# Optimization experiments

Hardware: AMD Instinct MI355X
Metric: run time of the kernel (lower is better)

Reference implementation:

```python
import jax, jax.numpy as jnp
import numpy as np

N = 200_000   # nodes
E = 6_400_000 # edges (avg degree 32)
G = 1024      # graphs in the batch
H = 8         # hidden dim


def setup_inputs() -> dict:
    key = jax.random.key(0)
    ks = jax.random.split(key, 13)
    x = jax.random.normal(ks[0], (N, 1), dtype=jnp.float32)
    edge_index = jax.random.randint(ks[1], (2, E), 0, N, dtype=jnp.int32)
    batch = jnp.sort(jax.random.randint(ks[2], (N,), 0, G, dtype=jnp.int32))
    s = 0.3
    params = dict(
        W1a=s * jax.random.normal(ks[3], (1, H), jnp.float32),
        b1a=jnp.zeros((H,), jnp.float32),
        W1b=s * jax.random.normal(ks[4], (H, H), jnp.float32),
        b1b=jnp.zeros((H,), jnp.float32),
        W2a=s * jax.random.normal(ks[5], (H, H), jnp.float32),
        b2a=jnp.zeros((H,), jnp.float32),
        W2b=s * jax.random.normal(ks[6], (H, H), jnp.float32),
        b2b=jnp.zeros((H,), jnp.float32),
        Wfc=s * jax.random.normal(ks[7], (H, 1), jnp.float32),
        bfc=jnp.zeros((1,), jnp.float32),
    )
    return dict(x=x, edge_index=edge_index, batch=batch, **params)


def _gin_layer(h, src, dst, Wa, ba, Wb, bb):
    # GINConv with eps=0: mlp(x_i + sum_{j->i} x_j); messages aggregated at dst=edge_index[1]
    agg = jax.ops.segment_sum(h[src], dst, num_segments=N)  # [N, d]
    z = h + agg
    z = jax.nn.relu(z @ Wa + ba)
    return z @ Wb + bb


def reference(x, edge_index, batch, W1a, b1a, W1b, b1b, W2a, b2a, W2b, b2b, Wfc, bfc):
    src, dst = edge_index[0], edge_index[1]
    h = _gin_layer(x, src, dst, W1a, b1a, W1b, b1b)   # [N, 8]
    h = jax.nn.elu(h)
    h = _gin_layer(h, src, dst, W2a, b2a, W2b, b2b)   # [N, 8]
    # global mean pool over graphs
    sums = jax.ops.segment_sum(h, batch, num_segments=G)                  # [G, 8]
    counts = jax.ops.segment_sum(jnp.ones((N,), h.dtype), batch, num_segments=G)
    pooled = sums / jnp.maximum(counts, 1.0)[:, None]
    out = jax.nn.sigmoid(pooled @ Wfc + bfc)          # [G, 1]
    return out.reshape(-1)
```

## Files before the change

### kernel.cpp

```cpp
#include <hip/hip_runtime.h>
#include <hip/hip_fp8.h>
#include <math.h>

#define H 8
#define NBLKA 256
#define BTH 1024
#define BSH 8
#define BCAP 9216
#define TS 1024
#define CAP 14336
#define SCAP 25600
#define POOLG 128

__device__ __forceinline__ unsigned f2fp8(float f) {
    __hip_fp8_e4m3 q(f);
    return (unsigned)q.__x;
}
__device__ __forceinline__ float fp8f(unsigned v) {
    __hip_fp8_e4m3 q;
    q.__x = (__hip_fp8_storage_t)v;
    return (float)q;
}
__device__ __forceinline__ void acc8(float* a, uint2 v) {
    a[0] += fp8f(v.x & 255u);         a[1] += fp8f((v.x >> 8) & 255u);
    a[2] += fp8f((v.x >> 16) & 255u); a[3] += fp8f(v.x >> 24);
    a[4] += fp8f(v.y & 255u);         a[5] += fp8f((v.y >> 8) & 255u);
    a[6] += fp8f((v.y >> 16) & 255u); a[7] += fp8f(v.y >> 24);
}

__global__ __launch_bounds__(BTH) void scatterK(const int* __restrict__ ei, int E, int NB,
                                                int chunk, int* __restrict__ cursor,
                                                unsigned* __restrict__ packed) {
    __shared__ unsigned ss[SCAP];
    __shared__ int cnt[1024], sc[1024], base[1024], cur[1024];
    int t = threadIdx.x, blk = blockIdx.x;
    cnt[t] = 0;
    __syncthreads();
    int s = blk * chunk, e = min(E, s + chunk);
    for (int i = s + t; i < e; i += BTH)
        atomicAdd(&cnt[__builtin_nontemporal_load(ei + E + i) >> BSH], 1);
    __syncthreads();
    int c = cnt[t];
    sc[t] = c;
    __syncthreads();
    for (int off = 1; off < 1024; off <<= 1) {
        int v = (t >= off) ? sc[t - off] : 0;
        __syncthreads();
        sc[t] += v;
        __syncthreads();
    }
    cur[t] = sc[t] - c;
    base[t] = (t < NB && c > 0) ? atomicAdd(&cursor[t], c) : 0;
    __syncthreads();
    for (int i = s + t; i < e; i += BTH) {
        int src = __builtin_nontemporal_load(ei + i);
        int dst = __builtin_nontemporal_load(ei + E + i);
        int pos = atomicAdd(&cur[dst >> BSH], 1);
        ss[pos] = ((unsigned)src << 8) | (unsigned)(dst & 255);
    }
    __syncthreads();
    int wave = t >> 6, lane = t & 63;
    for (int j = wave; j < NB; j += (BTH >> 6)) {
        int n = cnt[j];
        int ls = sc[j] - n;
        int bs = base[j];
        int m = min(n, BCAP - bs);
        int gs = j * BCAP + bs;
        for (int k = lane; k < m; k += 64)
            packed[gs + k] = ss[ls + k];
    }
}

__global__ void sortL1K(unsigned* __restrict__ packed, const int* __restrict__ bucketCnt,
                        const float* __restrict__ x, int N,
                        const float* __restrict__ W1a, const float* __restrict__ b1a,
                        const float* __restrict__ W1b, const float* __restrict__ b1b,
                        int* __restrict__ nodeStart, uint2* __restrict__ h1) {
    __shared__ unsigned ss[CAP];
    __shared__ int cnt[256], sb[256], cur[256];
    __shared__ float sW1a[H], sb1a[H], sW1b[H * H], sb1b[H];
    int t = threadIdx.x, b = blockIdx.x;
    if (t < 256) cnt[t] = 0;
    else if (t < 256 + H) { int j = t - 256; sW1a[j] = W1a[j]; sb1a[j] = b1a[j]; sb1b[j] = b1b[j]; }
    else if (t < 256 + H + H * H) { int j = t - 256 - H; sW1b[j] = W1b[j]; }
    __syncthreads();
    int s = b * BCAP;
    int n_e = min(bucketCnt[b], BCAP);
    for (int i = t; i < n_e; i += TS)
        atomicAdd(&cnt[__builtin_nontemporal_load(packed + s + i) & 255u], 1);
    __syncthreads();
    if (t < 256) sb[t] = cnt[t];
    __syncthreads();
    for (int off = 1; off < 256; off <<= 1) {
        int add = (t < 256 && t >= off) ? sb[t - off] : 0;
        __syncthreads();
        if (t < 256) sb[t] += add;
        __syncthreads();
    }
    if (t < 256) {
        int excl = sb[t] - cnt[t];
        cur[t] = excl;
        nodeStart[(b << BSH) + t] = s + excl;
    }
    __syncthreads();
    for (int i = t; i < n_e; i += TS) {
        unsigned p = __builtin_nontemporal_load(packed + s + i);
        int pos = atomicAdd(&cur[p & 255u], 1);
        ss[pos] = p >> 8;
    }
    __syncthreads();
    for (int i = t; i < n_e; i += TS) packed[s + i] = ss[i];
    int node = t >> 2, q4 = t & 3;
    int gn = (b << BSH) + node;
    int lo = sb[node] - cnt[node], hi = sb[node];
    float sum = 0.f;
    for (int k = lo + q4; k < hi; k += 16) {
        int k1 = k + 4, k2 = k + 8, k3 = k + 12;
        unsigned i0 = ss[k];
        unsigned i1 = ss[min(k1, hi - 1)];
        unsigned i2 = ss[min(k2, hi - 1)];
        unsigned i3 = ss[min(k3, hi - 1)];
        float x0 = x[i0], x1 = x[i1], x2 = x[i2], x3 = x[i3];
        sum += x0;
        if (k1 < hi) sum += x1;
        if (k2 < hi) sum += x2;
        if (k3 < hi) sum += x3;
    }
    sum += __shfl_xor(sum, 1, 64);
    sum += __shfl_xor(sum, 2, 64);
    if (q4 == 0 && gn < N) {
        float z = x[gn] + sum;
        float tv[H];
#pragma unroll
        for (int k = 0; k < H; k++) tv[k] = fmaxf(fmaf(z, sW1a[k], sb1a[k]), 0.f);
        float hv[H];
#pragma unroll
        for (int j = 0; j < H; j++) {
            float a = sb1b[j];
#pragma unroll
            for (int k = 0; k < H; k++) a += tv[k] * sW1b[k * H + j];
            hv[j] = a > 0.f ? a : (expf(a) - 1.f);
        }
        uint2 o;
        o.x = f2fp8(hv[0]) | (f2fp8(hv[1]) << 8) | (f2fp8(hv[2]) << 16) | (f2fp8(hv[3]) << 24);
        o.y = f2fp8(hv[4]) | (f2fp8(hv[5]) << 8) | (f2fp8(hv[6]) << 16) | (f2fp8(hv[7]) << 24);
        h1[gn] = o;
    }
}

__global__ __launch_bounds__(1024) void layer2K(
        const unsigned* __restrict__ packed, const int* __restrict__ nodeStart,
        const int* __restrict__ bucketCnt, const uint2* __restrict__ h1, int N,
        const float* __restrict__ W2a, const float* __restrict__ b2a,
        const float* __restrict__ W2b, const float* __restrict__ b2b,
        const int* __restrict__ batch, float* __restrict__ sumsCnt) {
    __shared__ unsigned ss[BCAP];
    __shared__ int sNS[257];
    __shared__ float pool[POOLG * 9];
    __shared__ float sW2a[H * H], sb2a[H], sW2b[H * H], sb2b[H];
    int t = threadIdx.x, b = blockIdx.x;
    int s = b * BCAP;
    int n_e = min(bucketCnt[b], BCAP);
    for (int i = t; i < n_e; i += 1024)
        ss[i] = __builtin_nontemporal_load(packed + s + i);
    if (t < 256) sNS[t] = nodeStart[(b << BSH) + t] - s;
    if (t == 256) sNS[256] = 0;
    if (t < H) { sb2a[t] = b2a[t]; sb2b[t] = b2b[t]; }
    else if (t >= 64 && t < 64 + H * H) sW2a[t - 64] = W2a[t - 64];
    else if (t >= 192 && t < 192 + H * H) sW2b[t - 192] = W2b[t - 192];
    __syncthreads();
    if (t == 0) sNS[256] = n_e;
    __syncthreads();
    int node = t >> 2, q4 = t & 3;
    int gn = (b << BSH) + node;
    int lo = sNS[node], hi = sNS[node + 1];
    float a[H] = {0.f, 0.f, 0.f, 0.f, 0.f, 0.f, 0.f, 0.f};
    for (int k = lo + q4; k < hi; k += 16) {
        int k1 = k + 4, k2 = k + 8, k3 = k + 12;
        unsigned i0 = ss[k];
        unsigned i1 = ss[min(k1, hi - 1)];
        unsigned i2 = ss[min(k2, hi - 1)];
        unsigned i3 = ss[min(k3, hi - 1)];
        uint2 v0 = h1[i0];
        uint2 v1 = h1[i1];
        uint2 v2 = h1[i2];
        uint2 v3 = h1[i3];
        acc8(a, v0);
        if (k1 < hi) acc8(a, v1);
        if (k2 < hi) acc8(a, v2);
        if (k3 < hi) acc8(a, v3);
    }
#pragma unroll
    for (int j = 0; j < H; j++) {
        a[j] += __shfl_xor(a[j], 1, 64);
        a[j] += __shfl_xor(a[j], 2, 64);
    }
    bool valid = (q4 == 0) && (gn < N);
    float h2[H];
    int g = 0;
    if (valid) {
        uint2 v = h1[gn];
        float z[H] = {fp8f(v.x & 255u) + a[0],         fp8f((v.x >> 8) & 255u) + a[1],
                      fp8f((v.x >> 16) & 255u) + a[2], fp8f(v.x >> 24) + a[3],
                      fp8f(v.y & 255u) + a[4],         fp8f((v.y >> 8) & 255u) + a[5],
                      fp8f((v.y >> 16) & 255u) + a[6], fp8f(v.y >> 24) + a[7]};
        float tv[H];
#pragma unroll
        for (int k = 0; k < H; k++) {
            float acc = sb2a[k];
#pragma unroll
            for (int j = 0; j < H; j++) acc += z[j] * sW2a[j * H + k];
            tv[k] = fmaxf(acc, 0.f);
        }
#pragma unroll
        for (int j = 0; j < H; j++) {
            float acc = sb2b[j];
#pragma unroll
            for (int k = 0; k < H; k++) acc += tv[k] * sW2b[k * H + j];
            h2[j] = acc;
        }
        g = batch[gn];
    }
    int gfirst = batch[min(b << BSH, N - 1)];
    int glast  = batch[min((b << BSH) + 255, N - 1)];
    int span = glast - gfirst + 1;
    if (span <= POOLG) {
        int span9 = span * 9;
        for (int j = t; j < span9; j += 1024) pool[j] = 0.f;
        __syncthreads();
        if (valid) {
            float* p = &pool[(g - gfirst) * 9];
#pragma unroll
            for (int j = 0; j < H; j++) atomicAdd(p + j, h2[j]);
            atomicAdd(p + 8, 1.f);
        }
        __syncthreads();
        for (int j = t; j < span9; j += 1024)
            atomicAdd(&sumsCnt[(size_t)gfirst * 9 + j], pool[j]);
    } else if (valid) {
        float* p = &sumsCnt[(size_t)g * 9];
#pragma unroll
        for (int j = 0; j < H; j++) atomicAdd(p + j, h2[j]);
        atomicAdd(p + 8, 1.f);
    }
}

__global__ void finalK(const float* __restrict__ sumsCnt, const float* __restrict__ Wfc,
                       const float* __restrict__ bfc, float* __restrict__ out, int G) {
    int g = blockIdx.x * blockDim.x + threadIdx.x;
    if (g >= G) return;
    const float* s = &sumsCnt[(size_t)g * 9];
    float c = fmaxf(s[8], 1.f);
    float dot = 0.f;
#pragma unroll
    for (int j = 0; j < H; j++) dot += s[j] * Wfc[j];
    float a = dot / c + bfc[0];
    out[g] = 1.f / (1.f + expf(-a));
}

__global__ void edge_agg1(const int* __restrict__ ei, const float* __restrict__ x,
                          float* __restrict__ agg1, int E) {
    int e = blockIdx.x * blockDim.x + threadIdx.x;
    if (e >= E) return;
    atomicAdd(&agg1[ei[E + e]], x[ei[e]]);
}
__global__ void node1F(const float* __restrict__ x, const float* __restrict__ agg1,
                       const float* __restrict__ W1a, const float* __restrict__ b1a,
                       const float* __restrict__ W1b, const float* __restrict__ b1b,
                       float* __restrict__ h1, int N) {
    int n = blockIdx.x * blockDim.x + threadIdx.x;
    if (n >= N) return;
    float z = x[n] + agg1[n];
    float tv[H];
#pragma unroll
    for (int k = 0; k < H; k++) tv[k] = fmaxf(z * W1a[k] + b1a[k], 0.f);
#pragma unroll
    for (int j = 0; j < H; j++) {
        float acc = b1b[j];
#pragma unroll
        for (int k = 0; k < H; k++) acc += tv[k] * W1b[k * H + j];
        h1[(size_t)n * H + j] = acc > 0.f ? acc : (expf(acc) - 1.f);
    }
}
__global__ void edge_agg2(const int* __restrict__ ei, const float* __restrict__ h1,
                          float* __restrict__ agg2, int E) {
    long long i = (long long)blockIdx.x * blockDim.x + threadIdx.x;
    if (i >= (long long)E * H) return;
    int e = (int)(i >> 3), k = (int)(i & 7);
    atomicAdd(&agg2[(size_t)ei[E + e] * H + k], h1[(size_t)ei[e] * H + k]);
}
__global__ void node2F(const float* __restrict__ h1, const float* __restrict__ agg2,
                       const float* __restrict__ W2a, const float* __restrict__ b2a,
                       const float* __restrict__ W2b, const float* __restrict__ b2b,
                       const int* __restrict__ batch,
                       float* __restrict__ sums, float* __restrict__ counts, int N) {
    int n = blockIdx.x * blockDim.x + threadIdx.x;
    if (n >= N) return;
    float z[H], tv[H];
#pragma unroll
    for (int j = 0; j < H; j++) z[j] = h1[(size_t)n * H + j] + agg2[(size_t)n * H + j];
#pragma unroll
    for (int k = 0; k < H; k++) {
        float a = b2a[k];
#pragma unroll
        for (int j = 0; j < H; j++) a += z[j] * W2a[j * H + k];
        tv[k] = fmaxf(a, 0.f);
    }
    int g = batch[n];
#pragma unroll
    for (int j = 0; j < H; j++) {
        float a = b2b[j];
#pragma unroll
        for (int k = 0; k < H; k++) a += tv[k] * W2b[k * H + j];
        atomicAdd(&sums[(size_t)g * H + j], a);
    }
    atomicAdd(&counts[g], 1.f);
}
__global__ void finalF(const float* __restrict__ sums, const float* __restrict__ counts,
                       const float* __restrict__ Wfc, const float* __restrict__ bfc,
                       float* __restrict__ out, int G) {
    int g = blockIdx.x * blockDim.x + threadIdx.x;
    if (g >= G) return;
    float c = fmaxf(counts[g], 1.f);
    float acc = bfc[0];
#pragma unroll
    for (int j = 0; j < H; j++) acc += (sums[(size_t)g * H + j] / c) * Wfc[j];
    out[g] = 1.f / (1.f + expf(-acc));
}

extern "C" void kernel_launch(void* const* d_in, const int* in_sizes, int n_in,
                              void* d_out, int out_size, void* d_ws, size_t ws_size,
                              hipStream_t stream) {
    const float* x    = (const float*)d_in[0];
    const int*   ei   = (const int*)d_in[1];
    const int*   batch= (const int*)d_in[2];
    const float* W1a  = (const float*)d_in[3];
    const float* b1a  = (const float*)d_in[4];
    const float* W1b  = (const float*)d_in[5];
    const float* b1b  = (const float*)d_in[6];
    const float* W2a  = (const float*)d_in[7];
    const float* b2a  = (const float*)d_in[8];
    const float* W2b  = (const float*)d_in[9];
    const float* b2b  = (const float*)d_in[10];
    const float* Wfc  = (const float*)d_in[11];
    const float* bfc  = (const float*)d_in[12];

    const int N = in_sizes[0];
    const int E = in_sizes[1] / 2;
    const int G = out_size;
    const int NB = (N + 255) >> BSH;
    const int chunk = (E + NBLKA - 1) / NBLKA;
    const int B = 256;

    auto rnd4 = [](size_t v) { return (v + 3) & ~(size_t)3; };
    size_t o_cur  = 0;
    size_t o_sc   = 1024;
    size_t zelems = o_sc + (size_t)9 * G;
    size_t o_ns   = rnd4(zelems);
    size_t o_h1   = rnd4(o_ns + ((size_t)NB << BSH) + 1);
    size_t o_pk   = rnd4(o_h1 + ((size_t)NB << BSH) * 2);
    size_t total  = o_pk + (size_t)NB * BCAP;

    bool srcFits = (N <= (1 << 18));
    bool chunkFits = (chunk <= SCAP);
    bool capOK = ((size_t)E / NB) * 10 <= (size_t)BCAP * 9;
    if (NB <= 1024 && srcFits && chunkFits && capOK && ws_size >= total * 4) {
        int*      wsi = (int*)d_ws;
        float*    wsf = (float*)d_ws;
        unsigned* wsu = (unsigned*)d_ws;
        int*      cursor    = wsi + o_cur;
        float*    sumsCnt   = wsf + o_sc;
        int*      nodeStart = wsi + o_ns;
        uint2*    h1        = (uint2*)(wsu + o_h1);
        unsigned* packed    = wsu + o_pk;

        hipMemsetAsync(d_ws, 0, zelems * 4, stream);
        scatterK<<<NBLKA, BTH, 0, stream>>>(ei, E, NB, chunk, cursor, packed);
        sortL1K<<<NB, TS, 0, stream>>>(packed, cursor, x, N, W1a, b1a, W1b, b1b,
                                       nodeStart, h1);
        layer2K<<<NB, 1024, 0, stream>>>(packed, nodeStart, cursor, h1, N,
                                         W2a, b2a, W2b, b2b, batch, sumsCnt);
        finalK<<<(G + B - 1) / B, B, 0, stream>>>(sumsCnt, Wfc, bfc, (float*)d_out, G);
    } else {
        float* ws     = (float*)d_ws;
        float* agg1   = ws;
        float* agg2   = agg1 + (size_t)N;
        float* sums   = agg2 + (size_t)8 * N;
        float* counts = sums + (size_t)8 * G;
        float* h1     = counts + (size_t)G;
        hipMemsetAsync(ws, 0, ((size_t)9 * N + (size_t)9 * G) * sizeof(float), stream);
        edge_agg1<<<(E + B - 1) / B, B, 0, stream>>>(ei, x, agg1, E);
        node1F<<<(N + B - 1) / B, B, 0, stream>>>(x, agg1, W1a, b1a, W1b, b1b, h1, N);
        long long tot = (long long)E * H;
        edge_agg2<<<(int)((tot + B - 1) / B), B, 0, stream>>>(ei, h1, agg2, E);
        node2F<<<(N + B - 1) / B, B, 0, stream>>>(h1, agg2, W2a, b2a, W2b, b2b, batch,
                                                  sums, counts, N);
        finalF<<<(G + B - 1) / B, B, 0, stream>>>(sums, counts, Wfc, bfc, (float*)d_out, G);
    }
}
```

Baseline: 262.6 us.

## Stage edge data in LDS to avoid second global pass in scatter and sort

scatterK now reads each edge's src/dst from global memory once, stores the packed word and bucket id in shared memory, and reuses them in the placement pass instead of re-reading global memory. The block count doubles so the per-block chunk fits the new shared buffers. sortL1K likewise caches the bucket's packed entries in LDS on the counting pass rather than reloading them. This removes one global read pass per kernel but raises shared-memory use per block, which may lower occupancy.

Measured after the change: 271.2 us. 3.3% more time.

```diff
diff --git a/kernel.cpp b/kernel.cpp
--- a/kernel.cpp
+++ b/kernel.cpp
@@ -3,13 +3,12 @@
 #include <math.h>
 
 #define H 8
-#define NBLKA 256
+#define NBLKA 512
 #define BTH 1024
+#define SCHK 12544
 #define BSH 8
 #define BCAP 9216
 #define TS 1024
-#define CAP 14336
-#define SCAP 25600
 #define POOLG 128
 
 __device__ __forceinline__ unsigned f2fp8(float f) {
@@ -31,14 +30,23 @@
 __global__ __launch_bounds__(BTH) void scatterK(const int* __restrict__ ei, int E, int NB,
                                                 int chunk, int* __restrict__ cursor,
                                                 unsigned* __restrict__ packed) {
-    __shared__ unsigned ss[SCAP];
+    __shared__ unsigned pk[SCHK];
+    __shared__ unsigned short bk[SCHK];
+    __shared__ unsigned ss[SCHK];
     __shared__ int cnt[1024], sc[1024], base[1024], cur[1024];
     int t = threadIdx.x, blk = blockIdx.x;
     cnt[t] = 0;
     __syncthreads();
     int s = blk * chunk, e = min(E, s + chunk);
-    for (int i = s + t; i < e; i += BTH)
-        atomicAdd(&cnt[__builtin_nontemporal_load(ei + E + i) >> BSH], 1);
+    int n = e - s;
+    for (int i = t; i < n; i += BTH) {
+        int src = __builtin_nontemporal_load(ei + s + i);
+        int dst = __builtin_nontemporal_load(ei + E + s + i);
+        int b = dst >> BSH;
+        pk[i] = ((unsigned)src << 8) | (unsigned)(dst & 255);
+        bk[i] = (unsigned short)b;
+        atomicAdd(&cnt[b], 1);
+    }
     __syncthreads();
     int c = cnt[t];
     sc[t] = c;
@@ -52,19 +60,17 @@
     cur[t] = sc[t] - c;
     base[t] = (t < NB && c > 0) ? atomicAdd(&cursor[t], c) : 0;
     __syncthreads();
-    for (int i = s + t; i < e; i += BTH) {
-        int src = __builtin_nontemporal_load(ei + i);
-        int dst = __builtin_nontemporal_load(ei + E + i);
-        int pos = atomicAdd(&cur[dst >> BSH], 1);
-        ss[pos] = ((unsigned)src << 8) | (unsigned)(dst & 255);
+    for (int i = t; i < n; i += BTH) {
+        int pos = atomicAdd(&cur[bk[i]], 1);
+        ss[pos] = pk[i];
     }
     __syncthreads();
     int wave = t >> 6, lane = t & 63;
     for (int j = wave; j < NB; j += (BTH >> 6)) {
-        int n = cnt[j];
-        int ls = sc[j] - n;
+        int nj = cnt[j];
+        int ls = sc[j] - nj;
         int bs = base[j];
-        int m = min(n, BCAP - bs);
+        int m = min(nj, BCAP - bs);
         int gs = j * BCAP + bs;
         for (int k = lane; k < m; k += 64)
             packed[gs + k] = ss[ls + k];
@@ -76,7 +82,8 @@
                         const float* __restrict__ W1a, const float* __restrict__ b1a,
                         const float* __restrict__ W1b, const float* __restrict__ b1b,
                         int* __restrict__ nodeStart, uint2* __restrict__ h1) {
-    __shared__ unsigned ss[CAP];
+    __shared__ unsigned raw[BCAP];
+    __shared__ unsigned ss[BCAP];
     __shared__ int cnt[256], sb[256], cur[256];
     __shared__ float sW1a[H], sb1a[H], sW1b[H * H], sb1b[H];
     int t = threadIdx.x, b = blockIdx.x;
@@ -86,8 +93,11 @@
     __syncthreads();
     int s = b * BCAP;
     int n_e = min(bucketCnt[b], BCAP);
-    for (int i = t; i < n_e; i += TS)
-        atomicAdd(&cnt[__builtin_nontemporal_load(packed + s + i) & 255u], 1);
+    for (int i = t; i < n_e; i += TS) {
+        unsigned p = __builtin_nontemporal_load(packed + s + i);
+        raw[i] = p;
+        atomicAdd(&cnt[p & 255u], 1);
+    }
     __syncthreads();
     if (t < 256) sb[t] = cnt[t];
     __syncthreads();
@@ -104,7 +114,7 @@
     }
     __syncthreads();
     for (int i = t; i < n_e; i += TS) {
-        unsigned p = __builtin_nontemporal_load(packed + s + i);
+        unsigned p = raw[i];
         int pos = atomicAdd(&cur[p & 255u], 1);
         ss[pos] = p >> 8;
     }
@@ -362,7 +372,7 @@
     size_t total  = o_pk + (size_t)NB * BCAP;
 
     bool srcFits = (N <= (1 << 18));
-    bool chunkFits = (chunk <= SCAP);
+    bool chunkFits = (chunk <= SCHK);
     bool capOK = ((size_t)E / NB) * 10 <= (size_t)BCAP * 9;
     if (NB <= 1024 && srcFits && chunkFits && capOK && ws_size >= total * 4) {
         int*      wsi = (int*)d_ws;
```
